# Kernel optimization log

Hardware: AMD Instinct MI355X
Metric: run time of the kernel (lower is better)

The kernel has to match this reference:

```python
import jax, jax.numpy as jnp
import numpy as np

B, S, D, Fd, M, H, L = 4, 1024, 1024, 4096, 512, 16, 2
HD = D // H
EPS = 1e-5


def _ln(x, s, b):
    m = jnp.mean(x, axis=-1, keepdims=True)
    v = jnp.mean((x - m) ** 2, axis=-1, keepdims=True)
    return (x - m) * jax.lax.rsqrt(v + EPS) * s + b


def _mha(x, Wq, bq, Wk, bk, Wv, bv, Wo, bo):
    b_, s_, _ = x.shape
    Q = (x @ Wq + bq).reshape(b_, s_, H, HD)
    K = (x @ Wk + bk).reshape(b_, s_, H, HD)
    V = (x @ Wv + bv).reshape(b_, s_, H, HD)
    scores = jnp.einsum('bihd,bjhd->bhij', Q, K) / np.sqrt(HD).astype(np.float32)
    w = jax.nn.softmax(scores, axis=-1)
    out = jnp.einsum('bhij,bjhd->bihd', w, V).reshape(b_, s_, D)
    return out @ Wo + bo


def setup_inputs() -> dict:
    key = jax.random.key(0)
    ks = iter(jax.random.split(key, 40))
    w = lambda shape: jax.random.normal(next(ks), shape, jnp.float32) * 0.02
    inp = {
        'x': jax.random.normal(next(ks), (B, S, D), jnp.float32),
        # stacked per-global-layer params [L, ...]
        'Wq': w((L, D, D)), 'bq': jnp.zeros((L, D)),
        'Wk': w((L, D, D)), 'bk': jnp.zeros((L, D)),
        'Wv': w((L, D, D)), 'bv': jnp.zeros((L, D)),
        'Wo': w((L, D, D)), 'bo': jnp.zeros((L, D)),
        'W1': w((L, D, Fd)), 'b1': jnp.zeros((L, Fd)),
        'W2': w((L, Fd, D)), 'b2': jnp.zeros((L, D)),
        'n1s': jnp.ones((L, D)), 'n1b': jnp.zeros((L, D)),
        'n2s': jnp.ones((L, D)), 'n2b': jnp.zeros((L, D)),
        # top-level params
        'ln1s': jnp.ones((D,)), 'ln1b': jnp.zeros((D,)),
        'ln2s': jnp.ones((D,)), 'ln2b': jnp.zeros((D,)),
        'ln3s': jnp.ones((D,)), 'ln3b': jnp.zeros((D,)),
        'Wb': w((D, M)), 'bb': jnp.zeros((M,)),      # backbone stand-in
        'Wm': w((M, D)), 'bm': jnp.zeros((D,)),      # self.linear
        'Wf1': w((D, Fd)), 'bf1': jnp.zeros((Fd,)),  # top feed_forward
        'Wf2': w((Fd, D)), 'bf2': jnp.zeros((D,)),
    }
    return inp


def reference(x, Wq, bq, Wk, bk, Wv, bv, Wo, bo, W1, b1, W2, b2,
              n1s, n1b, n2s, n2b, ln1s, ln1b, ln2s, ln2b, ln3s, ln3b,
              Wb, bb, Wm, bm, Wf1, bf1, Wf2, bf2):
    # dropout is identity (eval mode)
    # global branch: stacked EncoderLayers
    g = x
    for i in range(L):
        a = _mha(g, Wq[i], bq[i], Wk[i], bk[i], Wv[i], bv[i], Wo[i], bo[i])
        g = _ln(g + a, n1s[i], n1b[i])
        ff = jax.nn.relu(g @ W1[i] + b1[i]) @ W2[i] + b2[i]
        g = _ln(g + ff, n2s[i], n2b[i])

    def local(frac):
        st = S // frac
        xs = x[:, -st:, :]
        mo = (xs @ Wb + bb) @ Wm + bm
        y = _ln(xs + mo, ln1s, ln1b)
        return jnp.pad(y, ((0, 0), (S - st, 0), (0, 0)))

    output = g + local(2) + local(4)  # S >= 4 branch
    h = _ln(output + x, ln2s, ln2b)
    ff = jax.nn.relu(output @ Wf1 + bf1) @ Wf2 + bf2
    return _ln(h + ff, ln3s, ln3b)
```

## Files before the change

### kernel.cpp

```cpp
#include <hip/hip_runtime.h>
#include <stdint.h>


typedef short   s16x8 __attribute__((ext_vector_type(8)));
typedef float   f32x4 __attribute__((ext_vector_type(4)));
typedef uint16_t u16x8 __attribute__((ext_vector_type(8)));
typedef uint16_t u16x4 __attribute__((ext_vector_type(4)));

__device__ __forceinline__ float bf2f(uint16_t h) {
    union { uint32_t u; float f; } c; c.u = ((uint32_t)h) << 16; return c.f;
}
__device__ __forceinline__ uint16_t f2bf(float f) {
    union { float f; uint32_t u; } c; c.f = f;
    uint32_t u = c.u;
    u += 0x7fffu + ((u >> 16) & 1u);
    return (uint16_t)(u >> 16);
}
__device__ __forceinline__ uint32_t cvt_pk_bf16(float lo, float hi) {
    uint32_t r;
    asm("v_cvt_pk_bf16_f32 %0, %1, %2" : "=v"(r) : "v"(lo), "v"(hi));
    return r;
}

__device__ __forceinline__ void g2l16(const uint16_t* g, uint16_t* l) {
    __builtin_amdgcn_global_load_lds(
        (const __attribute__((address_space(1))) void*)g,
        (__attribute__((address_space(3))) void*)l, 16, 0, 0);
}

template<int MODE>
__global__ __launch_bounds__(256, 2) void gemm128n(
    const uint16_t* __restrict__ A, const uint16_t* __restrict__ Bt,
    const float* __restrict__ bias0, const float* __restrict__ bias1,
    const float* __restrict__ bias2,
    uint16_t* __restrict__ C0, uint16_t* __restrict__ C1,
    uint16_t* __restrict__ C2,
    int N)
{
    __shared__ __align__(16) uint16_t smem[36864];
    uint16_t* sA = smem;
    uint16_t* sB = smem + 12288;

    const int t    = threadIdx.x;
    const int w    = t >> 6;
    const int lane = t & 63;
    const int qd   = lane >> 4;
    const int cc   = lane & 15;
    const int wn   = w * 64;

    const int id  = blockIdx.x;
    const int loc = id >> 3;
    const int bm  = (id & 7) * 4 + (loc & 3);
    const int bn  = loc >> 2;
    const int m0  = bm * 128;
    const int n0  = bn * 256;

    const float* bp = bias0;
    int n0c = n0;
    if (MODE == 3) {
        int seg = n0 >> 10;
        n0c = n0 & 1023;
        bp = (seg == 0) ? bias0 : (seg == 1) ? bias1 : bias2;
    }
    float bb[4];
#pragma unroll
    for (int j = 0; j < 4; ++j) bb[j] = bp[n0c + wn + j * 16 + cc];

    int offA[8], offB[4];
#pragma unroll
    for (int i = 0; i < 8; ++i) {
        int ml = i * 16 + cc;
        offA[i] = ml * 32 + ((qd ^ ((ml >> 1) & 3)) * 8);
    }
#pragma unroll
    for (int j = 0; j < 4; ++j) {
        int nl = wn + j * 16 + cc;
        offB[j] = nl * 32 + ((qd ^ ((nl >> 1) & 3)) * 8);
    }

    const uint16_t* pA[2]; int ldA[2];
#pragma unroll
    for (int is = 0; is < 2; ++is) {
        int gc = is * 256 + t;
        int row = gc >> 2, ph = gc & 3;
        pA[is]  = A + (size_t)(m0 + row) * 1024 + (ph ^ ((row >> 1) & 3)) * 8;
        ldA[is] = (is * 256 + w * 64) * 8;
    }
    const uint16_t* pB[4]; int ldB[4];
#pragma unroll
    for (int is = 0; is < 4; ++is) {
        int gc = is * 256 + t;
        int row = gc >> 2, ph = gc & 3;
        pB[is]  = Bt + (size_t)(n0 + row) * 1024 + (ph ^ ((row >> 1) & 3)) * 8;
        ldB[is] = (is * 256 + w * 64) * 8;
    }
    auto stage = [&](int tt, int slot) {
        int kt = tt * 32;
        uint16_t* dA = sA + slot * 4096;
        uint16_t* dB = sB + slot * 8192;
#pragma unroll
        for (int is = 0; is < 2; ++is) g2l16(pA[is] + kt, dA + ldA[is]);
#pragma unroll
        for (int is = 0; is < 4; ++is) g2l16(pB[is] + kt, dB + ldB[is]);
    };

    f32x4 acc[8][4];
#pragma unroll
    for (int i = 0; i < 8; ++i)
#pragma unroll
        for (int j = 0; j < 4; ++j) acc[i][j] = (f32x4)0.0f;

    stage(0, 0); stage(1, 1);
    asm volatile("s_waitcnt vmcnt(6)" ::: "memory");
    __builtin_amdgcn_s_barrier();

    int cur = 0, pf = 2;
#pragma unroll 1
    for (int kt = 0; kt < 32; ++kt) {
        const uint16_t* sa = sA + cur * 4096;
        const uint16_t* sb = sB + cur * 8192;
        s16x8 av[8], bv[4];
#pragma unroll
        for (int j = 0; j < 4; ++j) bv[j] = *(const s16x8*)(sb + offB[j]);
#pragma unroll
        for (int i = 0; i < 8; ++i) av[i] = *(const s16x8*)(sa + offA[i]);
        if (kt < 30) stage(kt + 2, pf);
        asm volatile("s_waitcnt lgkmcnt(0)" ::: "memory");
        __builtin_amdgcn_sched_barrier(0);
        __builtin_amdgcn_s_setprio(1);
#pragma unroll
        for (int i = 0; i < 8; ++i)
#pragma unroll
            for (int j = 0; j < 4; ++j)
                acc[i][j] = __builtin_amdgcn_mfma_f32_16x16x32_bf16(
                    av[i], bv[j], acc[i][j], 0, 0, 0);
        __builtin_amdgcn_s_setprio(0);
        if (kt < 30)       { asm volatile("s_waitcnt vmcnt(6)" ::: "memory"); }
        else if (kt == 30) { asm volatile("s_waitcnt vmcnt(0)" ::: "memory"); }
        __builtin_amdgcn_s_barrier();
        pf = cur;
        cur = (cur == 2) ? 0 : cur + 1;
    }

    if (MODE == 3 && (n0 >> 10) == 2) {
#pragma unroll
        for (int j = 0; j < 4; ++j) {
            int c = n0c + wn + j * 16 + cc;
            int hh = c >> 6, d = c & 63;
#pragma unroll
            for (int i = 0; i < 8; ++i) {
                int rb = m0 + i * 16 + qd * 4;
                int b = rb >> 10, s = rb & 1023;
                u16x4 o;
#pragma unroll
                for (int r = 0; r < 4; ++r) o[r] = f2bf(acc[i][j][r] + bb[j]);
                *(u16x4*)(C2 + ((size_t)((b * 16 + hh) * 64 + d)) * 1024 + s) = o;
            }
        }
        return;
    }
    {
        uint16_t* C = C0;
        int Nc = N;
        if (MODE == 3) {
            int seg = n0 >> 10;
            C = (seg == 0) ? C0 : C1;
            Nc = 1024;
        }
        constexpr int ST = 264;
#pragma unroll
        for (int i = 0; i < 8; ++i)
#pragma unroll
            for (int j = 0; j < 4; ++j) {
                f32x4 v = acc[i][j];
#pragma unroll
                for (int r = 0; r < 4; ++r) {
                    float val = v[r] + bb[j];
                    if (MODE == 1) val = fmaxf(val, 0.0f);
                    smem[(i * 16 + qd * 4 + r) * ST + wn + j * 16 + cc] = f2bf(val);
                }
            }
        __syncthreads();
#pragma unroll
        for (int p = 0; p < 16; ++p) {
            int row  = p * 8 + (t >> 5);
            int colc = (t & 31) * 8;
            u16x8 v = *(const u16x8*)(smem + row * ST + colc);
            *(u16x8*)(C + (size_t)(m0 + row) * Nc + n0c + colc) = v;
        }
    }
}

template<int MODE, int BN, int BK>
__global__ __launch_bounds__(256, 2) void gemm_bt(
    const uint16_t* __restrict__ A, const uint16_t* __restrict__ Bt,
    const float* __restrict__ bias0, const float* __restrict__ bias1,
    const float* __restrict__ bias2,
    uint16_t* __restrict__ C0, uint16_t* __restrict__ C1,
    uint16_t* __restrict__ C2,
    int M, int N, int K)
{
    constexpr int JN    = BN / 32;
    constexpr int KS    = BK / 32;
    constexpr int CPR   = BK / 8;
    constexpr int LG    = (BK == 32) ? 2 : 3;
    constexpr int RA    = (128 * BK / 8) / 256;
    constexpr int RB    = (BN  * BK / 8) / 256;
    constexpr int SLOTA = 128 * BK;
    constexpr int SLOTB = BN * BK;
    constexpr int STG   = 3 * (SLOTA + SLOTB);
    constexpr int EPI   = (MODE == 3) ? 0 : 128 * (BN + 8);
    constexpr int SMEM  = (STG > EPI) ? STG : EPI;
    __shared__ __align__(16) uint16_t smem[SMEM];
    uint16_t* sA = smem;
    uint16_t* sB = smem + 3 * SLOTA;

    const int t    = threadIdx.x;
    const int w    = t >> 6;
    const int lane = t & 63;
    const int qd   = lane >> 4;
    const int cc   = lane & 15;

    int bm, bn;
    {
        int gx = gridDim.x, gy = gridDim.y;
        if ((gy & 7) == 0) {
            int id   = blockIdx.y * gx + blockIdx.x;
            int gpg  = gy >> 3;
            int rest = id >> 3;
            bm = (id & 7) * gpg + rest % gpg;
            bn = rest / gpg;
        } else { bm = blockIdx.y; bn = blockIdx.x; }
    }
    const int m0 = bm * 128;
    const int n0 = bn * BN;
    const int wm = (w >> 1) * 64;
    const int wn = (w & 1) * (BN / 2);

    auto key = [](int row) -> int {
        return (BK == 32) ? ((row >> 1) & 3) : (row & 7);
    };

    f32x4 acc[4][JN];
#pragma unroll
    for (int i = 0; i < 4; ++i)
#pragma unroll
        for (int j = 0; j < JN; ++j) acc[i][j] = (f32x4)0.0f;

    int rA[RA], kA[RA];
#pragma unroll
    for (int is = 0; is < RA; ++is) {
        int gc = is * 256 + t;
        int row = gc >> LG, ph = gc & (CPR - 1);
        rA[is] = row;
        kA[is] = (ph ^ key(row)) * 8;
    }
    int rB[RB], kB[RB];
#pragma unroll
    for (int is = 0; is < RB; ++is) {
        int gc = is * 256 + t;
        int row = gc >> LG, ph = gc & (CPR - 1);
        rB[is] = row;
        kB[is] = (ph ^ key(row)) * 8;
    }
    int offA[4][KS], offB[JN][KS];
#pragma unroll
    for (int i = 0; i < 4; ++i) {
        int ml = wm + i * 16 + cc;
#pragma unroll
        for (int ks = 0; ks < KS; ++ks)
            offA[i][ks] = ml * BK + ((ks * 4 + qd) ^ key(ml)) * 8;
    }
#pragma unroll
    for (int j = 0; j < JN; ++j) {
        int nl = wn + j * 16 + cc;
#pragma unroll
        for (int ks = 0; ks < KS; ++ks)
            offB[j][ks] = nl * BK + ((ks * 4 + qd) ^ key(nl)) * 8;
    }

    auto stage = [&](int kt, int slot) {
#pragma unroll
        for (int is = 0; is < RA; ++is)
            g2l16(A + (size_t)(m0 + rA[is]) * K + kt + kA[is],
                  sA + (size_t)slot * SLOTA + (size_t)(is * 256 + w * 64) * 8);
#pragma unroll
        for (int is = 0; is < RB; ++is)
            g2l16(Bt + (size_t)(n0 + rB[is]) * K + kt + kB[is],
                  sB + (size_t)slot * SLOTB + (size_t)(is * 256 + w * 64) * 8);
    };

    const int NT = K / BK;
    stage(0, 0); stage(BK, 1);
    asm volatile("s_waitcnt vmcnt(6)" ::: "memory");
    __builtin_amdgcn_s_barrier();

    int cur = 0, pf = 2;
#pragma unroll 1
    for (int tt = 0; tt < NT; ++tt) {
        const uint16_t* sa = sA + cur * SLOTA;
        const uint16_t* sb = sB + cur * SLOTB;
        s16x8 af[KS][4], bv[KS][JN];
#pragma unroll
        for (int ks = 0; ks < KS; ++ks) {
#pragma unroll
            for (int j = 0; j < JN; ++j) bv[ks][j] = *(const s16x8*)(sb + offB[j][ks]);
#pragma unroll
            for (int i = 0; i < 4; ++i)  af[ks][i] = *(const s16x8*)(sa + offA[i][ks]);
        }
        if (tt + 2 < NT) stage((tt + 2) * BK, pf);
        asm volatile("s_waitcnt lgkmcnt(0)" ::: "memory");
        __builtin_amdgcn_sched_barrier(0);
        __builtin_amdgcn_s_setprio(1);
#pragma unroll
        for (int ks = 0; ks < KS; ++ks)
#pragma unroll
            for (int i = 0; i < 4; ++i)
#pragma unroll
                for (int j = 0; j < JN; ++j)
                    acc[i][j] = __builtin_amdgcn_mfma_f32_16x16x32_bf16(
                        af[ks][i], bv[ks][j], acc[i][j], 0, 0, 0);
        __builtin_amdgcn_s_setprio(0);
        if (tt + 2 < NT)      { asm volatile("s_waitcnt vmcnt(6)" ::: "memory"); }
        else if (tt + 2 == NT){ asm volatile("s_waitcnt vmcnt(0)" ::: "memory"); }
        __builtin_amdgcn_s_barrier();
        pf = cur;
        cur = (cur == 2) ? 0 : cur + 1;
    }

    if (MODE == 3) {
#pragma unroll
        for (int j = 0; j < JN; ++j) {
            int col = n0 + wn + j * 16 + cc;
            int seg = col >> 10;
            const float* bp = (seg == 0) ? bias0 : (seg == 1) ? bias1 : bias2;
            float bb = bp[col & 1023];
#pragma unroll
            for (int i = 0; i < 4; ++i) {
                f32x4 v = acc[i][j];
#pragma unroll
                for (int r = 0; r < 4; ++r) {
                    float val = v[r] + bb;
                    int row = m0 + wm + i * 16 + qd * 4 + r;
                    if (col < 1024) {
                        C0[(size_t)row * 1024 + col] = f2bf(val);
                    } else if (col < 2048) {
                        C1[(size_t)row * 1024 + (col - 1024)] = f2bf(val);
                    } else {
                        int c = col - 2048;
                        int b = row >> 10, s = row & 1023;
                        int hh = c >> 6, d = c & 63;
                        C2[((size_t)(b * 16 + hh) * 64 + d) * 1024 + s] = f2bf(val);
                    }
                }
            }
        }
    } else {
        constexpr int ST = BN + 8;
#pragma unroll
        for (int j = 0; j < JN; ++j) {
            int col = wn + j * 16 + cc;
            float bb = bias0[n0 + col];
#pragma unroll
            for (int i = 0; i < 4; ++i) {
                f32x4 v = acc[i][j];
#pragma unroll
                for (int r = 0; r < 4; ++r) {
                    float val = v[r] + bb;
                    if (MODE == 1) val = fmaxf(val, 0.0f);
                    smem[(wm + i * 16 + qd * 4 + r) * ST + col] = f2bf(val);
                }
            }
        }
        __syncthreads();
        constexpr int NP  = 128 * BN / 2048;
        constexpr int TPR = BN / 8;
#pragma unroll
        for (int p = 0; p < NP; ++p) {
            int row  = p * (256 / TPR) + t / TPR;
            int colc = (t % TPR) * 8;
            u16x8 v = *(const u16x8*)(smem + row * ST + colc);
            *(u16x8*)(C0 + (size_t)(m0 + row) * N + n0 + colc) = v;
        }
    }
}

#define FA_P 76
__global__ __launch_bounds__(256) void flash_attn(
    const uint16_t* __restrict__ Q, const uint16_t* __restrict__ K,
    const uint16_t* __restrict__ Vt, uint16_t* __restrict__ O)
{
    __shared__ __align__(16) uint16_t QPs[64 * FA_P];
    __shared__ __align__(16) uint16_t Ks[64 * FA_P];
    __shared__ __align__(16) uint16_t Vs[64 * FA_P];

    const int t    = threadIdx.x;
    const int w    = t >> 6;
    const int lane = t & 63;
    const int qd   = lane >> 4;
    const int cc   = lane & 15;
    const int id   = blockIdx.x;
    const int xg   = id & 7;
    const int loc  = id >> 3;
    const int bh   = xg * 8 + (loc >> 4);
    const int qblk = loc & 15;
    const int b    = bh >> 4, hh = bh & 15;
    const size_t rowbase = (size_t)b * 1024;

    int rr[2], ch8[2], lws[2];
    const uint16_t* Kp[2];
    const uint16_t* Vp[2];
#pragma unroll
    for (int is = 0; is < 2; ++is) {
        int c   = is * 256 + t;
        rr[is]  = c >> 3;
        ch8[is] = (c & 7) * 8;
        lws[is] = rr[is] * FA_P + ch8[is];
        Kp[is]  = K  + (rowbase + rr[is]) * 1024 + hh * 64 + ch8[is];
        Vp[is]  = Vt + ((size_t)(bh * 64 + rr[is])) * 1024 + ch8[is];
    }

    u16x8 kr[2], vr[2];
#pragma unroll
    for (int is = 0; is < 2; ++is) {
        kr[is] = *(const u16x8*)(Kp[is]);
        vr[is] = *(const u16x8*)(Vp[is]);
    }

#pragma unroll
    for (int is = 0; is < 2; ++is)
        *(u16x8*)(QPs + lws[is]) =
            *(const u16x8*)(Q + (rowbase + qblk * 64 + rr[is]) * 1024 + hh * 64 + ch8[is]);
    __syncthreads();
    s16x8 aq0 = *(const s16x8*)(QPs + (w * 16 + cc) * FA_P + qd * 8);
    s16x8 aq1 = *(const s16x8*)(QPs + (w * 16 + cc) * FA_P + 32 + qd * 8);
    __syncthreads();

    f32x4 o[4];
    float lrow[4] = {0.0f, 0.0f, 0.0f, 0.0f};
#pragma unroll
    for (int j = 0; j < 4; ++j) o[j] = (f32x4)0.0f;

#pragma unroll 1
    for (int kb = 64; kb <= 1024; kb += 64) {
#pragma unroll
        for (int is = 0; is < 2; ++is) {
            *(u16x8*)(Ks + lws[is]) = kr[is];
            *(u16x8*)(Vs + lws[is]) = vr[is];
        }
        if (kb < 1024) {
#pragma unroll
            for (int is = 0; is < 2; ++is) {
                kr[is] = *(const u16x8*)(Kp[is] + (size_t)kb * 1024);
                vr[is] = *(const u16x8*)(Vp[is] + kb);
            }
        }
        __syncthreads();

        f32x4 sc[4];
#pragma unroll
        for (int j = 0; j < 4; ++j) {
            s16x8 b0 = *(const s16x8*)(Ks + (j * 16 + cc) * FA_P + qd * 8);
            s16x8 b1 = *(const s16x8*)(Ks + (j * 16 + cc) * FA_P + 32 + qd * 8);
            sc[j] = __builtin_amdgcn_mfma_f32_16x16x32_bf16(aq0, b0, (f32x4)0.0f, 0, 0, 0);
            sc[j] = __builtin_amdgcn_mfma_f32_16x16x32_bf16(aq1, b1, sc[j], 0, 0, 0);
        }

#pragma unroll
        for (int r = 0; r < 4; ++r) {
            float p0 = __expf(sc[0][r] * 0.125f);
            float p1 = __expf(sc[1][r] * 0.125f);
            float p2 = __expf(sc[2][r] * 0.125f);
            float p3 = __expf(sc[3][r] * 0.125f);
            lrow[r] += (p0 + p1) + (p2 + p3);
            int prow = (w * 16 + qd * 4 + r) * FA_P + cc;
            uint32_t pk01 = cvt_pk_bf16(p0, p1);
            uint32_t pk23 = cvt_pk_bf16(p2, p3);
            QPs[prow]      = (uint16_t)pk01;
            QPs[prow + 16] = (uint16_t)(pk01 >> 16);
            QPs[prow + 32] = (uint16_t)pk23;
            QPs[prow + 48] = (uint16_t)(pk23 >> 16);
        }

#pragma unroll
        for (int ks = 0; ks < 2; ++ks) {
            s16x8 ap = *(const s16x8*)(QPs + (w * 16 + cc) * FA_P + ks * 32 + qd * 8);
#pragma unroll
            for (int j = 0; j < 4; ++j) {
                s16x8 bv = *(const s16x8*)(Vs + (j * 16 + cc) * FA_P + ks * 32 + qd * 8);
                o[j] = __builtin_amdgcn_mfma_f32_16x16x32_bf16(ap, bv, o[j], 0, 0, 0);
            }
        }
        __syncthreads();
    }

#pragma unroll
    for (int r = 0; r < 4; ++r) {
        float rs = lrow[r];
        rs += __shfl_xor(rs, 1);
        rs += __shfl_xor(rs, 2);
        rs += __shfl_xor(rs, 4);
        rs += __shfl_xor(rs, 8);
        float inv = 1.0f / rs;
        size_t grow = rowbase + qblk * 64 + w * 16 + qd * 4 + r;
#pragma unroll
        for (int j = 0; j < 4; ++j)
            O[grow * 1024 + hh * 64 + j * 16 + cc] = f2bf(o[j][r] * inv);
    }
}

template<int BT, int F32OUT>
__global__ __launch_bounds__(256) void ln_res(
    const uint16_t* __restrict__ A, const void* __restrict__ Bp,
    const float* __restrict__ S, const float* __restrict__ Bi,
    void* __restrict__ outp)
{
    const int row = blockIdx.x, t = threadIdx.x;
    const int w = t >> 6, lane = t & 63;
    u16x4 a4 = *(const u16x4*)(A + (size_t)row * 1024 + t * 4);
    float bvals[4];
    if (BT == 0) {
        u16x4 b4 = *(const u16x4*)((const uint16_t*)Bp + (size_t)row * 1024 + t * 4);
#pragma unroll
        for (int e = 0; e < 4; ++e) bvals[e] = bf2f(b4[e]);
    } else {
        float4 b4 = *(const float4*)((const float*)Bp + (size_t)row * 1024 + t * 4);
        bvals[0] = b4.x; bvals[1] = b4.y; bvals[2] = b4.z; bvals[3] = b4.w;
    }
    float v[4], sum = 0.0f, sq = 0.0f;
#pragma unroll
    for (int e = 0; e < 4; ++e) {
        v[e] = bf2f(a4[e]) + bvals[e];
        sum += v[e];
        sq  += v[e] * v[e];
    }
#pragma unroll
    for (int d = 1; d < 64; d <<= 1) {
        sum += __shfl_xor(sum, d);
        sq  += __shfl_xor(sq, d);
    }
    __shared__ float rs[4], rq[4];
    if (lane == 0) { rs[w] = sum; rq[w] = sq; }
    __syncthreads();
    sum = rs[0] + rs[1] + rs[2] + rs[3];
    sq  = rq[0] + rq[1] + rq[2] + rq[3];
    float mean = sum * (1.0f / 1024.0f);
    float var  = sq * (1.0f / 1024.0f) - mean * mean;
    float rstd = rsqrtf(var + 1e-5f);
    float4 s4  = *(const float4*)(S + t * 4);
    float4 bi4 = *(const float4*)(Bi + t * 4);
    float r0 = (v[0] - mean) * rstd * s4.x + bi4.x;
    float r1 = (v[1] - mean) * rstd * s4.y + bi4.y;
    float r2 = (v[2] - mean) * rstd * s4.z + bi4.z;
    float r3 = (v[3] - mean) * rstd * s4.w + bi4.w;
    if (F32OUT) {
        *(float4*)((float*)outp + (size_t)row * 1024 + t * 4) =
            make_float4(r0, r1, r2, r3);
    } else {
        u16x4 o4;
        o4[0] = f2bf(r0); o4[1] = f2bf(r1); o4[2] = f2bf(r2); o4[3] = f2bf(r3);
        *(u16x4*)((uint16_t*)outp + (size_t)row * 1024 + t * 4) = o4;
    }
}

__global__ __launch_bounds__(256) void add3_ln(
    uint16_t* __restrict__ g, const uint16_t* __restrict__ y2,
    const uint16_t* __restrict__ y4, const float* __restrict__ x,
    const float* __restrict__ S, const float* __restrict__ Bi,
    uint16_t* __restrict__ h)
{
    const int row = blockIdx.x, t = threadIdx.x;
    const int w = t >> 6, lane = t & 63;
    const int b = row >> 10, s = row & 1023;
    const size_t e = (size_t)row * 1024 + t * 4;
    u16x4 gv = *(const u16x4*)(g + e);
    float v[4];
#pragma unroll
    for (int k = 0; k < 4; ++k) v[k] = bf2f(gv[k]);
    if (s >= 512) {
        u16x4 a = *(const u16x4*)(y2 + ((size_t)(b * 512 + s - 512)) * 1024 + t * 4);
#pragma unroll
        for (int k = 0; k < 4; ++k) v[k] += bf2f(a[k]);
    }
    if (s >= 768) {
        u16x4 a = *(const u16x4*)(y4 + ((size_t)(b * 256 + s - 768)) * 1024 + t * 4);
#pragma unroll
        for (int k = 0; k < 4; ++k) v[k] += bf2f(a[k]);
    }
    u16x4 o4;
#pragma unroll
    for (int k = 0; k < 4; ++k) o4[k] = f2bf(v[k]);
    *(u16x4*)(g + e) = o4;

    float4 xv = *(const float4*)(x + e);
    float v2[4] = { v[0] + xv.x, v[1] + xv.y, v[2] + xv.z, v[3] + xv.w };
    float sum = 0.0f, sq = 0.0f;
#pragma unroll
    for (int k = 0; k < 4; ++k) { sum += v2[k]; sq += v2[k] * v2[k]; }
#pragma unroll
    for (int d = 1; d < 64; d <<= 1) {
        sum += __shfl_xor(sum, d);
        sq  += __shfl_xor(sq, d);
    }
    __shared__ float rs[4], rq[4];
    if (lane == 0) { rs[w] = sum; rq[w] = sq; }
    __syncthreads();
    sum = rs[0] + rs[1] + rs[2] + rs[3];
    sq  = rq[0] + rq[1] + rq[2] + rq[3];
    float mean = sum * (1.0f / 1024.0f);
    float var  = sq * (1.0f / 1024.0f) - mean * mean;
    float rstd = rsqrtf(var + 1e-5f);
    float4 s4  = *(const float4*)(S + t * 4);
    float4 bi4 = *(const float4*)(Bi + t * 4);
    u16x4 ho;
    ho[0] = f2bf((v2[0] - mean) * rstd * s4.x + bi4.x);
    ho[1] = f2bf((v2[1] - mean) * rstd * s4.y + bi4.y);
    ho[2] = f2bf((v2[2] - mean) * rstd * s4.z + bi4.z);
    ho[3] = f2bf((v2[3] - mean) * rstd * s4.w + bi4.w);
    *(u16x4*)(h + e) = ho;
}

__global__ __launch_bounds__(256) void copy_rows_f32(
    const float* __restrict__ x, uint16_t* __restrict__ out, int lgst)
{
    size_t e = ((size_t)blockIdx.x * 256 + threadIdx.x) * 4;
    int row = (int)(e >> 10), col = (int)(e & 1023);
    int st = 1 << lgst;
    int b = row >> lgst, s = row & (st - 1);
    float4 a = *(const float4*)(x + ((size_t)(b * 1024 + (1024 - st) + s)) * 1024 + col);
    u16x4 o4;
    o4[0] = f2bf(a.x); o4[1] = f2bf(a.y); o4[2] = f2bf(a.z); o4[3] = f2bf(a.w);
    *(u16x4*)(out + e) = o4;
}

__global__ __launch_bounds__(256) void transpose_k(
    const float* __restrict__ W0, const float* __restrict__ W1,
    const float* __restrict__ W2, uint16_t* __restrict__ Wt, int Kd, int Nd)
{
    const int z = blockIdx.z;
    const float* W = (z == 0) ? W0 : (z == 1) ? W1 : W2;
    uint16_t* dst = Wt + (size_t)z * Kd * Nd;
    __shared__ uint16_t tile[64][68];
    const int t  = threadIdx.x;
    const int n0 = blockIdx.x * 64, k0 = blockIdx.y * 64;
#pragma unroll
    for (int p = 0; p < 4; ++p) {
        int k  = p * 16 + (t >> 4);
        int nn = (t & 15) * 4;
        float4 a = *(const float4*)(W + (size_t)(k0 + k) * Nd + n0 + nn);
        tile[nn + 0][k] = f2bf(a.x);
        tile[nn + 1][k] = f2bf(a.y);
        tile[nn + 2][k] = f2bf(a.z);
        tile[nn + 3][k] = f2bf(a.w);
    }
    __syncthreads();
#pragma unroll
    for (int p = 0; p < 2; ++p) {
        int nn = p * 32 + (t >> 3);
        int kk = (t & 7) * 8;
        u16x8 o = *(const u16x8*)(&tile[nn][kk]);
        *(u16x8*)(dst + (size_t)(n0 + nn) * Kd + k0 + kk) = o;
    }
}

__global__ __launch_bounds__(256) void cvt(
    const float* __restrict__ src, uint16_t* __restrict__ dst)
{
    size_t i = ((size_t)blockIdx.x * 256 + threadIdx.x) * 8;
    float4 a = *(const float4*)(src + i);
    float4 b = *(const float4*)(src + i + 4);
    u16x8 o;
    o[0] = f2bf(a.x); o[1] = f2bf(a.y); o[2] = f2bf(a.z); o[3] = f2bf(a.w);
    o[4] = f2bf(b.x); o[5] = f2bf(b.y); o[6] = f2bf(b.z); o[7] = f2bf(b.w);
    *(u16x8*)(dst + i) = o;
}

extern "C" void kernel_launch(void* const* d_in, const int* in_sizes, int n_in,
                              void* d_out, int out_size, void* d_ws, size_t ws_size,
                              hipStream_t stream)
{
    const float* x    = (const float*)d_in[0];
    const float* Wq   = (const float*)d_in[1];
    const float* bq   = (const float*)d_in[2];
    const float* Wk   = (const float*)d_in[3];
    const float* bk   = (const float*)d_in[4];
    const float* Wv   = (const float*)d_in[5];
    const float* bv   = (const float*)d_in[6];
    const float* Wo   = (const float*)d_in[7];
    const float* bo   = (const float*)d_in[8];
    const float* W1   = (const float*)d_in[9];
    const float* b1   = (const float*)d_in[10];
    const float* W2   = (const float*)d_in[11];
    const float* b2   = (const float*)d_in[12];
    const float* n1s  = (const float*)d_in[13];
    const float* n1b  = (const float*)d_in[14];
    const float* n2s  = (const float*)d_in[15];
    const float* n2b  = (const float*)d_in[16];
    const float* ln1s = (const float*)d_in[17];
    const float* ln1b = (const float*)d_in[18];
    const float* ln2s = (const float*)d_in[19];
    const float* ln2b = (const float*)d_in[20];
    const float* ln3s = (const float*)d_in[21];
    const float* ln3b = (const float*)d_in[22];
    const float* Wb   = (const float*)d_in[23];
    const float* bb   = (const float*)d_in[24];
    const float* Wm   = (const float*)d_in[25];
    const float* bm   = (const float*)d_in[26];
    const float* Wf1  = (const float*)d_in[27];
    const float* bf1  = (const float*)d_in[28];
    const float* Wf2  = (const float*)d_in[29];
    const float* bf2  = (const float*)d_in[30];

    char* ws = (char*)d_ws;
    const size_t MB = (size_t)1 << 20;
    uint16_t* g    = (uint16_t*)(ws);
    uint16_t* tb   = (uint16_t*)(ws + 8 * MB);
    char*     big  = ws + 16 * MB;
    uint16_t* qb   = (uint16_t*)(big);
    uint16_t* kbuf = (uint16_t*)(big + 8 * MB);
    uint16_t* vtb  = (uint16_t*)(big + 16 * MB);
    uint16_t* ob   = (uint16_t*)(big + 24 * MB);
    uint16_t* ffb  = (uint16_t*)(big);
    uint16_t* xbf  = (uint16_t*)(ws + 48 * MB);
    uint16_t* hb   = (uint16_t*)(ws + 48 * MB);
    uint16_t* wT   = (uint16_t*)(ws + 56 * MB);

    auto T = [&](const float* Wsrc, int Kd, int Nd, uint16_t* dst) {
        transpose_k<<<dim3(Nd / 64, Kd / 64, 1), 256, 0, stream>>>(
            Wsrc, Wsrc, Wsrc, dst, Kd, Nd);
    };

    cvt<<<2048, 256, 0, stream>>>(x, xbf);

    const uint16_t* gin = xbf;
    for (int i = 0; i < 2; ++i) {
        const size_t wOff = (size_t)i * 1024 * 1024;
        const size_t fOff = (size_t)i * 1024 * 4096;
        transpose_k<<<dim3(16, 16, 3), 256, 0, stream>>>(
            Wq + wOff, Wk + wOff, Wv + wOff, wT, 1024, 1024);
        gemm128n<3><<<384, 256, 0, stream>>>(
            gin, wT, bq + i * 1024, bk + i * 1024, bv + i * 1024,
            qb, kbuf, vtb, 3072);
        flash_attn<<<1024, 256, 0, stream>>>(qb, kbuf, vtb, ob);
        T(Wo + wOff, 1024, 1024, wT);
        gemm_bt<0, 64, 64><<<dim3(16, 32), 256, 0, stream>>>(
            ob, wT, bo + i * 1024, nullptr, nullptr, tb, nullptr, nullptr,
            4096, 1024, 1024);
        ln_res<0, 0><<<4096, 256, 0, stream>>>(gin, tb, n1s + i * 1024, n1b + i * 1024, g);
        T(W1 + fOff, 1024, 4096, wT);
        gemm128n<1><<<512, 256, 0, stream>>>(
            g, wT, b1 + i * 4096, nullptr, nullptr, ffb, nullptr, nullptr, 4096);
        T(W2 + fOff, 4096, 1024, wT);
        gemm_bt<0, 64, 64><<<dim3(16, 32), 256, 0, stream>>>(
            ffb, wT, b2 + i * 1024, nullptr, nullptr, tb, nullptr, nullptr,
            4096, 1024, 4096);
        ln_res<0, 0><<<4096, 256, 0, stream>>>(g, tb, n2s + i * 1024, n2b + i * 1024, g);
        gin = g;
    }

    uint16_t* xsc = (uint16_t*)(big);
    uint16_t* lk  = (uint16_t*)(big + 8 * MB);
    uint16_t* mo  = (uint16_t*)(big + 16 * MB);
    uint16_t* yy  = (uint16_t*)(big + 24 * MB);
    copy_rows_f32<<<2048, 256, 0, stream>>>(x, xsc, 9);
    copy_rows_f32<<<1024, 256, 0, stream>>>(x, xsc + (size_t)2048 * 1024, 8);
    uint16_t* WbT = wT;
    uint16_t* WmT = wT + (size_t)512 * 1024;
    T(Wb, 1024, 512, WbT);
    T(Wm, 512, 1024, WmT);
    gemm_bt<0, 64, 64><<<dim3(8, 24), 256, 0, stream>>>(
        xsc, WbT, bb, nullptr, nullptr, lk, nullptr, nullptr, 3072, 512, 1024);
    gemm_bt<0, 64, 64><<<dim3(16, 24), 256, 0, stream>>>(
        lk, WmT, bm, nullptr, nullptr, mo, nullptr, nullptr, 3072, 1024, 512);
    ln_res<0, 0><<<3072, 256, 0, stream>>>(xsc, mo, ln1s, ln1b, yy);
    uint16_t* y2 = yy;
    uint16_t* y4 = yy + (size_t)2048 * 1024;

    add3_ln<<<4096, 256, 0, stream>>>(g, y2, y4, x, ln2s, ln2b, hb);
    T(Wf1, 1024, 4096, wT);
    gemm128n<1><<<512, 256, 0, stream>>>(
        g, wT, bf1, nullptr, nullptr, ffb, nullptr, nullptr, 4096);
    T(Wf2, 4096, 1024, wT);
    gemm_bt<0, 64, 64><<<dim3(16, 32), 256, 0, stream>>>(
        ffb, wT, bf2, nullptr, nullptr, tb, nullptr, nullptr, 4096, 1024, 4096);
    ln_res<0, 1><<<4096, 256, 0, stream>>>(hb, tb, ln3s, ln3b, d_out);
}
```

Baseline: 720.5 us.

## Process 128 query rows per flash-attention block to share K/V tiles across 8 waves

Doubles the flash attention block to 512 threads covering 128 query rows, so each K/V tile loaded into shared memory is reused by twice as many waves. This halves global K/V traffic and the per-block staging work, since each thread now loads one K and one V vector per iteration. In exchange the grid halves to 512 blocks, which may lower occupancy and balance across CUs, and shared memory per block grows.

```diff
diff --git a/kernel.cpp b/kernel.cpp
--- a/kernel.cpp
+++ b/kernel.cpp
@@ -386,11 +386,11 @@
 }
 
 #define FA_P 76
-__global__ __launch_bounds__(256) void flash_attn(
+__global__ __launch_bounds__(512) void flash_attn(
     const uint16_t* __restrict__ Q, const uint16_t* __restrict__ K,
     const uint16_t* __restrict__ Vt, uint16_t* __restrict__ O)
 {
-    __shared__ __align__(16) uint16_t QPs[64 * FA_P];
+    __shared__ __align__(16) uint16_t QPs[128 * FA_P];
     __shared__ __align__(16) uint16_t Ks[64 * FA_P];
     __shared__ __align__(16) uint16_t Vs[64 * FA_P];
 
@@ -402,35 +402,26 @@
     const int id   = blockIdx.x;
     const int xg   = id & 7;
     const int loc  = id >> 3;
-    const int bh   = xg * 8 + (loc >> 4);
-    const int qblk = loc & 15;
+    const int bh   = xg * 8 + (loc >> 3);
+    const int qp   = loc & 7;
     const int b    = bh >> 4, hh = bh & 15;
     const size_t rowbase = (size_t)b * 1024;
 
-    int rr[2], ch8[2], lws[2];
-    const uint16_t* Kp[2];
-    const uint16_t* Vp[2];
+    const int rK   = t >> 3;
+    const int ch8  = (t & 7) * 8;
+    const int lwsK = rK * FA_P + ch8;
+    const uint16_t* Kp = K  + (rowbase + rK) * 1024 + hh * 64 + ch8;
+    const uint16_t* Vp = Vt + ((size_t)(bh * 64 + rK)) * 1024 + ch8;
+
+    u16x8 kr = *(const u16x8*)(Kp);
+    u16x8 vr = *(const u16x8*)(Vp);
+
 #pragma unroll
     for (int is = 0; is < 2; ++is) {
-        int c   = is * 256 + t;
-        rr[is]  = c >> 3;
-        ch8[is] = (c & 7) * 8;
-        lws[is] = rr[is] * FA_P + ch8[is];
-        Kp[is]  = K  + (rowbase + rr[is]) * 1024 + hh * 64 + ch8[is];
-        Vp[is]  = Vt + ((size_t)(bh * 64 + rr[is])) * 1024 + ch8[is];
-    }
-
-    u16x8 kr[2], vr[2];
-#pragma unroll
-    for (int is = 0; is < 2; ++is) {
-        kr[is] = *(const u16x8*)(Kp[is]);
-        vr[is] = *(const u16x8*)(Vp[is]);
-    }
-
-#pragma unroll
-    for (int is = 0; is < 2; ++is)
-        *(u16x8*)(QPs + lws[is]) =
-            *(const u16x8*)(Q + (rowbase + qblk * 64 + rr[is]) * 1024 + hh * 64 + ch8[is]);
+        int c = is * 512 + t, r = c >> 3, ch = (c & 7) * 8;
+        *(u16x8*)(QPs + r * FA_P + ch) =
+            *(const u16x8*)(Q + (rowbase + qp * 128 + r) * 1024 + hh * 64 + ch);
+    }
     __syncthreads();
     s16x8 aq0 = *(const s16x8*)(QPs + (w * 16 + cc) * FA_P + qd * 8);
     s16x8 aq1 = *(const s16x8*)(QPs + (w * 16 + cc) * FA_P + 32 + qd * 8);
@@ -443,17 +434,11 @@
 
 #pragma unroll 1
     for (int kb = 64; kb <= 1024; kb += 64) {
-#pragma unroll
-        for (int is = 0; is < 2; ++is) {
-            *(u16x8*)(Ks + lws[is]) = kr[is];
-            *(u16x8*)(Vs + lws[is]) = vr[is];
-        }
+        *(u16x8*)(Ks + lwsK) = kr;
+        *(u16x8*)(Vs + lwsK) = vr;
         if (kb < 1024) {
-#pragma unroll
-            for (int is = 0; is < 2; ++is) {
-                kr[is] = *(const u16x8*)(Kp[is] + (size_t)kb * 1024);
-                vr[is] = *(const u16x8*)(Vp[is] + kb);
-            }
+            kr = *(const u16x8*)(Kp + (size_t)kb * 1024);
+            vr = *(const u16x8*)(Vp + kb);
         }
         __syncthreads();
 
@@ -502,7 +487,7 @@
         rs += __shfl_xor(rs, 4);
         rs += __shfl_xor(rs, 8);
         float inv = 1.0f / rs;
-        size_t grow = rowbase + qblk * 64 + w * 16 + qd * 4 + r;
+        size_t grow = rowbase + qp * 128 + w * 16 + qd * 4 + r;
 #pragma unroll
         for (int j = 0; j < 4; ++j)
             O[grow * 1024 + hh * 64 + j * 16 + cc] = f2bf(o[j][r] * inv);
@@ -741,7 +726,7 @@
         gemm128n<3><<<384, 256, 0, stream>>>(
             gin, wT, bq + i * 1024, bk + i * 1024, bv + i * 1024,
             qb, kbuf, vtb, 3072);
-        flash_attn<<<1024, 256, 0, stream>>>(qb, kbuf, vtb, ob);
+        flash_attn<<<512, 512, 0, stream>>>(qb, kbuf, vtb, ob);
         T(Wo + wOff, 1024, 1024, wT);
         gemm_bt<0, 64, 64><<<dim3(16, 32), 256, 0, stream>>>(
             ob, wT, bo + i * 1024, nullptr, nullptr, tb, nullptr, nullptr,
```

New measurement: 724.9 us. Within noise of the previous version (+0.6%).
